# Kernel tuning notes

Measured on AMD Instinct MI355X. Metric: run time of the kernel, lower is better.

## Reference

```python
import jax, jax.numpy as jnp
import numpy as np

STATE_DIM = 16
CHANNELS = 256
LENGTH = 8192
SAMPLE_RATE = 100.0


def setup_inputs() -> dict:
    key = jax.random.key(0)
    ks = jax.random.split(key, 4)
    fan = 1.0 / np.sqrt(CHANNELS)  # lecun-normal-ish scale, flax Dense default
    x = jax.random.normal(ks[0], (LENGTH, CHANNELS), dtype=jnp.float32)
    logA = jnp.log(1.0 + jnp.arange(STATE_DIM, dtype=jnp.float32))  # module's Ainit
    W_dt = jax.random.normal(ks[1], (CHANNELS, CHANNELS), dtype=jnp.float32) * fan
    b_dt = jnp.zeros((CHANNELS,), dtype=jnp.float32)
    W_B = jax.random.normal(ks[2], (CHANNELS, STATE_DIM), dtype=jnp.float32) * fan
    b_B = jnp.zeros((STATE_DIM,), dtype=jnp.float32)
    W_C = jax.random.normal(ks[3], (CHANNELS, STATE_DIM), dtype=jnp.float32) * fan
    b_C = jnp.zeros((STATE_DIM,), dtype=jnp.float32)
    return {"x": x, "logA": logA, "W_dt": W_dt, "b_dt": b_dt,
            "W_B": W_B, "b_B": b_B, "W_C": W_C, "b_C": b_C}


def reference(x, logA, W_dt, b_dt, W_B, b_B, W_C, b_C):
    # x: (L, C)
    A = -jnp.exp(logA)                                   # (S,)
    dt = jax.nn.softplus(1.0 / SAMPLE_RATE + x @ W_dt + b_dt)  # (L, C)
    B = 1.0 + x @ W_B + b_B                              # (L, S)
    C = x @ W_C + b_C                                    # (L, S)
    # discretize: Adiscr = exp(A * dt), shape (L, C, S)
    Adiscr = jnp.exp(dt[:, :, None] * A[None, None, :])
    # Bdiscr = exp((Adiscr - 1) * (B / A))  (faithful to source, incl. outer exp)
    Bdiscr = jnp.exp((Adiscr - 1.0) * (B / A)[:, None, :])  # (L, C, S)
    u = Bdiscr * x[:, :, None]                           # (L, C, S)

    def ssm_scan(p1, p2):
        (A1, c1), (A2, c2) = p1, p2
        return (A2 * A1, c2 + A2 * c1)

    _, h = jax.lax.associative_scan(ssm_scan, (Adiscr, u))  # h: (L, C, S)
    y = jnp.einsum('ls,lcs->lc', C, h)                    # (L, C)
    return y
```

## Files before the change

### kernel.cpp

```cpp
#include <hip/hip_runtime.h>
#include <hip/hip_bf16.h>
#include <math.h>

#define LL 8192
#define CC 256
#define SS 16
#define NJ (CC*SS)
#define GG 256
#define TT 32
#define SP 4
#define CB 64
#define SEGS 16
#define PER (GG/SEGS)

#define LOG2E 1.4426950408889634f
#define LN2   0.6931471805599453f

typedef __attribute__((ext_vector_type(8))) short short8;
typedef __attribute__((ext_vector_type(4))) float floatx4;

__device__ __forceinline__ float fexp2(float v){ return __builtin_amdgcn_exp2f(v); }
__device__ __forceinline__ float flog2v(float v){ return __builtin_amdgcn_logf(v); }

__device__ __forceinline__ float softplus(float z){
    float t = fexp2(-fabsf(z) * LOG2E);
    return fmaxf(z, 0.f) + LN2 * flog2v(1.f + t);
}

__device__ __forceinline__ unsigned short f2b(float f){
    __hip_bfloat16 h = __float2bfloat16(f);
    return *(unsigned short*)&h;
}
__device__ __forceinline__ float b2f(unsigned short u){
    __hip_bfloat16 h = *(__hip_bfloat16*)&u;
    return __bfloat162float(h);
}

#define MBM 64
#define MBN 32
#define MBK 64
#define ASTR 72

__global__ __launch_bounds__(256,4) void k_mm(
    const float* __restrict__ x,
    const float* __restrict__ Wdt, const float* __restrict__ WB,
    const float* __restrict__ WC,
    const float* __restrict__ bdt, const float* __restrict__ bB,
    const float* __restrict__ bC, const float* __restrict__ logA,
    float* __restrict__ dt, float* __restrict__ boa, float* __restrict__ cm)
{
    __shared__ unsigned short Ah[MBM*ASTR];
    __shared__ unsigned short Al[MBM*ASTR];
    __shared__ unsigned short Bh[MBN*ASTR];
    __shared__ unsigned short Bl[MBN*ASTR];

    const int tid  = threadIdx.x;
    const int row0 = blockIdx.x * MBM;
    const int n0   = blockIdx.y * MBN;

    const int lane = tid & 63;
    const int wv   = tid >> 6;
    const int wm   = wv >> 1;
    const int wn   = wv & 1;
    const int m16  = lane & 15;
    const int q    = lane >> 4;

    const int bn  = tid & 31;
    const int bkb = (tid >> 5) * 8;
    const int bcol = n0 + bn;
    const float* __restrict__ wp;
    int wstride;
    if (bcol < 256)      { wp = Wdt + bcol;       wstride = CC; }
    else if (bcol < 272) { wp = WB  + (bcol-256); wstride = SS; }
    else                 { wp = WC  + (bcol-272); wstride = SS; }

    floatx4 acc[2];
    acc[0] = (floatx4){0.f,0.f,0.f,0.f};
    acc[1] = (floatx4){0.f,0.f,0.f,0.f};

    for (int k0 = 0; k0 < CC; k0 += MBK) {
        __syncthreads();
        #pragma unroll
        for (int h2 = 0; h2 < 2; h2++){
            int chunk = tid + h2*256;
            int r    = chunk >> 3;
            int koff = (chunk & 7) * 8;
            float4 f0 = *(const float4*)&x[(size_t)(row0+r)*CC + k0 + koff];
            float4 f1 = *(const float4*)&x[(size_t)(row0+r)*CC + k0 + koff + 4];
            float fv[8] = {f0.x,f0.y,f0.z,f0.w,f1.x,f1.y,f1.z,f1.w};
            unsigned short hs[8], ls[8];
            #pragma unroll
            for (int i=0;i<8;i++){
                hs[i] = f2b(fv[i]);
                ls[i] = f2b(fv[i] - b2f(hs[i]));
            }
            uint4 ph, pl;
            ph.x = (unsigned)hs[0] | ((unsigned)hs[1] << 16);
            ph.y = (unsigned)hs[2] | ((unsigned)hs[3] << 16);
            ph.z = (unsigned)hs[4] | ((unsigned)hs[5] << 16);
            ph.w = (unsigned)hs[6] | ((unsigned)hs[7] << 16);
            pl.x = (unsigned)ls[0] | ((unsigned)ls[1] << 16);
            pl.y = (unsigned)ls[2] | ((unsigned)ls[3] << 16);
            pl.z = (unsigned)ls[4] | ((unsigned)ls[5] << 16);
            pl.w = (unsigned)ls[6] | ((unsigned)ls[7] << 16);
            *(uint4*)&Ah[r*ASTR + koff] = ph;
            *(uint4*)&Al[r*ASTR + koff] = pl;
        }
        {
            unsigned short hs[8], ls[8];
            #pragma unroll
            for (int i=0;i<8;i++){
                float v = wp[(size_t)(k0 + bkb + i)*wstride];
                hs[i] = f2b(v);
                ls[i] = f2b(v - b2f(hs[i]));
            }
            uint4 ph, pl;
            ph.x = (unsigned)hs[0] | ((unsigned)hs[1] << 16);
            ph.y = (unsigned)hs[2] | ((unsigned)hs[3] << 16);
            ph.z = (unsigned)hs[4] | ((unsigned)hs[5] << 16);
            ph.w = (unsigned)hs[6] | ((unsigned)hs[7] << 16);
            pl.x = (unsigned)ls[0] | ((unsigned)ls[1] << 16);
            pl.y = (unsigned)ls[2] | ((unsigned)ls[3] << 16);
            pl.z = (unsigned)ls[4] | ((unsigned)ls[5] << 16);
            pl.w = (unsigned)ls[6] | ((unsigned)ls[7] << 16);
            *(uint4*)&Bh[bn*ASTR + bkb] = ph;
            *(uint4*)&Bl[bn*ASTR + bkb] = pl;
        }
        __syncthreads();

        #pragma unroll
        for (int ks = 0; ks < MBK; ks += 32) {
            short8 bh = *(const short8*)&Bh[(wn*16 + m16)*ASTR + ks + q*8];
            short8 bl = *(const short8*)&Bl[(wn*16 + m16)*ASTR + ks + q*8];
            #pragma unroll
            for (int mt = 0; mt < 2; mt++){
                short8 ah = *(const short8*)&Ah[(wm*32 + mt*16 + m16)*ASTR + ks + q*8];
                short8 al = *(const short8*)&Al[(wm*32 + mt*16 + m16)*ASTR + ks + q*8];
                acc[mt] = __builtin_amdgcn_mfma_f32_16x16x32_bf16(al, bh, acc[mt], 0, 0, 0);
                acc[mt] = __builtin_amdgcn_mfma_f32_16x16x32_bf16(ah, bl, acc[mt], 0, 0, 0);
                acc[mt] = __builtin_amdgcn_mfma_f32_16x16x32_bf16(ah, bh, acc[mt], 0, 0, 0);
            }
        }
    }

    const int col = n0 + wn*16 + m16;
    if (col < 256) {
        float bias = bdt[col];
        #pragma unroll
        for (int mt = 0; mt < 2; mt++){
            #pragma unroll
            for (int r = 0; r < 4; r++){
                int row = row0 + wm*32 + mt*16 + q*4 + r;
                dt[(size_t)row*CC + col] = softplus(0.01f + acc[mt][r] + bias);
            }
        }
    } else if (col < 272) {
        int s = col - 256;
        float A = -fexp2(logA[s] * LOG2E);
        float sc = LOG2E / A;
        float bias = bB[s];
        #pragma unroll
        for (int mt = 0; mt < 2; mt++){
            #pragma unroll
            for (int r = 0; r < 4; r++){
                int row = row0 + wm*32 + mt*16 + q*4 + r;
                boa[(size_t)row*SS + s] = (1.f + acc[mt][r] + bias) * sc;
            }
        }
    } else {
        int s = col - 272;
        float bias = bC[s];
        #pragma unroll
        for (int mt = 0; mt < 2; mt++){
            #pragma unroll
            for (int r = 0; r < 4; r++){
                int row = row0 + wm*32 + mt*16 + q*4 + r;
                cm[(size_t)row*SS + s] = acc[mt][r] + bias;
            }
        }
    }
}

__global__ __launch_bounds__(256) void k_scan1(const float* __restrict__ dt,
    const float* __restrict__ x, const float* __restrict__ boa,
    const float* __restrict__ logA,
    float* __restrict__ Ap, float* __restrict__ Hl)
{
    const int tid = threadIdx.x;
    const int sg  = tid & 3;
    const int cl  = tid >> 2;
    const int g   = blockIdx.x;
    const int c   = blockIdx.y * CB + cl;
    const int row0 = g * TT;

    float Al2[SP];
    #pragma unroll
    for (int i=0;i<SP;i++) Al2[i] = -fexp2(logA[sg*SP+i]*LOG2E) * LOG2E;

    const float* __restrict__ dp = dt  + (size_t)row0*CC + c;
    const float* __restrict__ xp = x   + (size_t)row0*CC + c;
    const float* __restrict__ bp = boa + (size_t)row0*SS + sg*SP;

    float Apr[SP], h[SP];
    #pragma unroll
    for (int i=0;i<SP;i++){ Apr[i]=1.f; h[i]=0.f; }

    #pragma unroll 8
    for (int t=0;t<TT;t++){
        float d  = dp[(size_t)t*CC];
        float xv = xp[(size_t)t*CC];
        float4 bo = *(const float4*)&bp[(size_t)t*SS];
        float bov[SP] = {bo.x, bo.y, bo.z, bo.w};
        #pragma unroll
        for (int s=0;s<SP;s++){
            float a = fexp2(d * Al2[s]);
            float u = fexp2(fmaf(a, bov[s], -bov[s])) * xv;
            h[s] = fmaf(a, h[s], u);
            Apr[s] *= a;
        }
    }

    const size_t base = (size_t)g*NJ + (size_t)c*SS + sg*SP;
    *(float4*)&Ap[base] = make_float4(Apr[0],Apr[1],Apr[2],Apr[3]);
    *(float4*)&Hl[base] = make_float4(h[0],h[1],h[2],h[3]);
}

__global__ __launch_bounds__(256) void k_carry(const float* __restrict__ Ap,
    const float* __restrict__ Hl, float* __restrict__ Cr)
{
    const int tid = threadIdx.x;
    const int jl  = tid & 15;
    const int seg = tid >> 4;
    const int j   = blockIdx.x * 16 + jl;

    const size_t base = (size_t)(seg*PER)*NJ + j;

    float a[PER], u[PER];
    #pragma unroll
    for (int k=0;k<PER;k++){
        a[k] = Ap[base + (size_t)k*NJ];
        u[k] = Hl[base + (size_t)k*NJ];
    }
    float Aag = 1.f, Uag = 0.f;
    #pragma unroll
    for (int k=0;k<PER;k++){ Uag = fmaf(a[k], Uag, u[k]); Aag *= a[k]; }

    __shared__ float As[SEGS][17], Us[SEGS][17];
    As[seg][jl] = Aag; Us[seg][jl] = Uag;
    __syncthreads();
    float hin = 0.f;
    for (int t = 0; t < seg; ++t)
        hin = fmaf(As[t][jl], hin, Us[t][jl]);

    float h = hin;
    #pragma unroll
    for (int k=0;k<PER;k++){
        Cr[base + (size_t)k*NJ] = h;
        h = fmaf(a[k], h, u[k]);
    }
}

__global__ __launch_bounds__(256) void k_scan2(const float* __restrict__ dt,
    const float* __restrict__ x, const float* __restrict__ boa,
    const float* __restrict__ cmat, const float* __restrict__ logA,
    const float* __restrict__ Cr, float* __restrict__ y)
{
    const int tid = threadIdx.x;
    const int sg  = tid & 3;
    const int cl  = tid >> 2;
    const int g   = blockIdx.x;
    const int c   = blockIdx.y * CB + cl;
    const int row0 = g * TT;

    float Al2[SP];
    #pragma unroll
    for (int i=0;i<SP;i++) Al2[i] = -fexp2(logA[sg*SP+i]*LOG2E) * LOG2E;

    const float* __restrict__ dp = dt   + (size_t)row0*CC + c;
    const float* __restrict__ xp = x    + (size_t)row0*CC + c;
    const float* __restrict__ bp = boa  + (size_t)row0*SS + sg*SP;
    const float* __restrict__ cp = cmat + (size_t)row0*SS + sg*SP;
    float* __restrict__ yp = y + (size_t)row0*CC + c;

    float h[SP];
    {
        float4 hc = *(const float4*)&Cr[(size_t)g*NJ + (size_t)c*SS + sg*SP];
        h[0]=hc.x; h[1]=hc.y; h[2]=hc.z; h[3]=hc.w;
    }

    #pragma unroll 8
    for (int t=0;t<TT;t++){
        float d  = dp[(size_t)t*CC];
        float xv = xp[(size_t)t*CC];
        float4 bo = *(const float4*)&bp[(size_t)t*SS];
        float4 cv = *(const float4*)&cp[(size_t)t*SS];
        float bov[SP] = {bo.x,bo.y,bo.z,bo.w};
        float cvv[SP] = {cv.x,cv.y,cv.z,cv.w};
        float yv = 0.f;
        #pragma unroll
        for (int s=0;s<SP;s++){
            float a = fexp2(d * Al2[s]);
            float u = fexp2(fmaf(a, bov[s], -bov[s])) * xv;
            h[s] = fmaf(a, h[s], u);
            yv = fmaf(cvv[s], h[s], yv);
        }
        yv += __shfl_xor(yv, 1);
        yv += __shfl_xor(yv, 2);
        if (sg == 0) yp[(size_t)t*CC] = yv;
    }
}

extern "C" void kernel_launch(void* const* d_in, const int* in_sizes, int n_in,
                              void* d_out, int out_size, void* d_ws, size_t ws_size,
                              hipStream_t stream) {
    const float* x    = (const float*)d_in[0];
    const float* logA = (const float*)d_in[1];
    const float* W_dt = (const float*)d_in[2];
    const float* b_dt = (const float*)d_in[3];
    const float* W_B  = (const float*)d_in[4];
    const float* b_B  = (const float*)d_in[5];
    const float* W_C  = (const float*)d_in[6];
    const float* b_C  = (const float*)d_in[7];
    float* y  = (float*)d_out;
    float* ws = (float*)d_ws;

    float* dt   = ws;
    float* boa  = dt   + (size_t)LL*CC;
    float* cmv  = boa  + (size_t)LL*SS;
    float* Ap   = cmv  + (size_t)LL*SS;
    float* Hl   = Ap   + (size_t)GG*NJ;
    float* Cr   = Hl   + (size_t)GG*NJ;

    hipLaunchKernelGGL(k_mm,   dim3(128,9), dim3(256), 0, stream,
                       x, W_dt, W_B, W_C, b_dt, b_B, b_C, logA, dt, boa, cmv);
    hipLaunchKernelGGL(k_scan1, dim3(GG,4), dim3(256), 0, stream,
                       dt, x, boa, logA, Ap, Hl);
    hipLaunchKernelGGL(k_carry, dim3(NJ/16), dim3(256), 0, stream, Ap, Hl, Cr);
    hipLaunchKernelGGL(k_scan2, dim3(GG,4), dim3(256), 0, stream,
                       dt, x, boa, cmv, logA, Cr, y);
}
```

Measured before the change: 121.7 us.

## Fuse projection GEMM, chunk scans and carry into one cooperative kernel

Replaces the four launches (GEMM, chunk scan, carry propagation, output scan) with a single cooperative kernel of 256 blocks. Each block computes its 32-row slice of dt, B and C into shared memory and never writes them to global memory. Grid-wide syncs separate the chunk scan, carry and final scan phases. This removes the global round trips for dt/boa/cm and the launch gaps, but every block now reconverts all of W into bf16 hi/lo (a 256-fold redundant weight conversion), uses large shared memory, and runs only 256 blocks.

```diff
diff --git a/kernel.cpp b/kernel.cpp
--- a/kernel.cpp
+++ b/kernel.cpp
@@ -1,5 +1,6 @@
 #include <hip/hip_runtime.h>
 #include <hip/hip_bf16.h>
+#include <hip/hip_cooperative_groups.h>
 #include <math.h>
 
 #define LL 8192
@@ -8,13 +9,16 @@
 #define NJ (CC*SS)
 #define GG 256
 #define TT 32
-#define SP 4
-#define CB 64
+#define THREADS 512
 #define SEGS 16
 #define PER (GG/SEGS)
 
 #define LOG2E 1.4426950408889634f
 #define LN2   0.6931471805599453f
+
+#define XSTR 264
+#define WSTR 264
+#define DSTR 260
 
 typedef __attribute__((ext_vector_type(8))) short short8;
 typedef __attribute__((ext_vector_type(4))) float floatx4;
@@ -36,277 +40,228 @@
     return __bfloat162float(h);
 }
 
-#define MBM 64
-#define MBN 32
-#define MBK 64
-#define ASTR 72
-
-__global__ __launch_bounds__(256,4) void k_mm(
-    const float* __restrict__ x,
-    const float* __restrict__ Wdt, const float* __restrict__ WB,
-    const float* __restrict__ WC,
-    const float* __restrict__ bdt, const float* __restrict__ bB,
-    const float* __restrict__ bC, const float* __restrict__ logA,
-    float* __restrict__ dt, float* __restrict__ boa, float* __restrict__ cm)
+__global__ __launch_bounds__(THREADS, 2) void k_fused(
+    const float* __restrict__ x, const float* __restrict__ logA,
+    const float* __restrict__ Wdt, const float* __restrict__ bdt,
+    const float* __restrict__ WB,  const float* __restrict__ bB,
+    const float* __restrict__ WC,  const float* __restrict__ bC,
+    float* __restrict__ Ap, float* __restrict__ Hl, float* __restrict__ Cr,
+    float* __restrict__ y)
 {
-    __shared__ unsigned short Ah[MBM*ASTR];
-    __shared__ unsigned short Al[MBM*ASTR];
-    __shared__ unsigned short Bh[MBN*ASTR];
-    __shared__ unsigned short Bl[MBN*ASTR];
+    __shared__ unsigned short xh[32*XSTR];
+    __shared__ unsigned short xl[32*XSTR];
+    __shared__ unsigned short Wh2[64*WSTR];
+    __shared__ unsigned short Wl2[64*WSTR];
+    __shared__ float dtS[32*DSTR];
+    __shared__ float boaS[32*SS];
+    __shared__ float cmS[32*SS];
+    __shared__ float As[SEGS][17], Us[SEGS][17];
 
     const int tid  = threadIdx.x;
-    const int row0 = blockIdx.x * MBM;
-    const int n0   = blockIdx.y * MBN;
+    const int g    = blockIdx.x;
+    const int row0 = g * TT;
+
+    #pragma unroll
+    for (int j = 0; j < 4; j++){
+        int idx = tid + j*THREADS;
+        int r   = idx >> 6;
+        int kq  = (idx & 63) * 4;
+        float4 f = *(const float4*)&x[(size_t)(row0+r)*CC + kq];
+        float fv[4] = {f.x, f.y, f.z, f.w};
+        unsigned short hs[4], ls[4];
+        #pragma unroll
+        for (int i=0;i<4;i++){ hs[i]=f2b(fv[i]); ls[i]=f2b(fv[i]-b2f(hs[i])); }
+        uint2 ph, pl;
+        ph.x = (unsigned)hs[0] | ((unsigned)hs[1] << 16);
+        ph.y = (unsigned)hs[2] | ((unsigned)hs[3] << 16);
+        pl.x = (unsigned)ls[0] | ((unsigned)ls[1] << 16);
+        pl.y = (unsigned)ls[2] | ((unsigned)ls[3] << 16);
+        *(uint2*)&xh[r*XSTR + kq] = ph;
+        *(uint2*)&xl[r*XSTR + kq] = pl;
+    }
 
     const int lane = tid & 63;
     const int wv   = tid >> 6;
-    const int wm   = wv >> 1;
-    const int wn   = wv & 1;
     const int m16  = lane & 15;
     const int q    = lane >> 4;
-
-    const int bn  = tid & 31;
-    const int bkb = (tid >> 5) * 8;
-    const int bcol = n0 + bn;
-    const float* __restrict__ wp;
-    int wstride;
-    if (bcol < 256)      { wp = Wdt + bcol;       wstride = CC; }
-    else if (bcol < 272) { wp = WB  + (bcol-256); wstride = SS; }
-    else                 { wp = WC  + (bcol-272); wstride = SS; }
-
-    floatx4 acc[2];
-    acc[0] = (floatx4){0.f,0.f,0.f,0.f};
-    acc[1] = (floatx4){0.f,0.f,0.f,0.f};
-
-    for (int k0 = 0; k0 < CC; k0 += MBK) {
+    const int mi   = wv & 1;
+    const int ni   = wv >> 1;
+
+    const int cw = tid & 63;
+    const int kb = (tid >> 6) * 32;
+
+    for (int nt = 0; nt < 5; nt++){
+        {
+            int bcol = nt*64 + cw;
+            const float* wp = nullptr; int wstr = 0;
+            if (bcol < 256)      { wp = Wdt + bcol;       wstr = CC; }
+            else if (bcol < 272) { wp = WB  + (bcol-256); wstr = SS; }
+            else if (bcol < 288) { wp = WC  + (bcol-272); wstr = SS; }
+            if (wp){
+                #pragma unroll
+                for (int i8 = 0; i8 < 32; i8 += 8){
+                    unsigned short hs[8], ls[8];
+                    #pragma unroll
+                    for (int u = 0; u < 8; u++){
+                        float v = wp[(size_t)(kb+i8+u)*wstr];
+                        hs[u] = f2b(v);
+                        ls[u] = f2b(v - b2f(hs[u]));
+                    }
+                    uint4 ph, pl;
+                    ph.x = (unsigned)hs[0] | ((unsigned)hs[1] << 16);
+                    ph.y = (unsigned)hs[2] | ((unsigned)hs[3] << 16);
+                    ph.z = (unsigned)hs[4] | ((unsigned)hs[5] << 16);
+                    ph.w = (unsigned)hs[6] | ((unsigned)hs[7] << 16);
+                    pl.x = (unsigned)ls[0] | ((unsigned)ls[1] << 16);
+                    pl.y = (unsigned)ls[2] | ((unsigned)ls[3] << 16);
+                    pl.z = (unsigned)ls[4] | ((unsigned)ls[5] << 16);
+                    pl.w = (unsigned)ls[6] | ((unsigned)ls[7] << 16);
+                    *(uint4*)&Wh2[cw*WSTR + kb + i8] = ph;
+                    *(uint4*)&Wl2[cw*WSTR + kb + i8] = pl;
+                }
+            }
+        }
         __syncthreads();
-        #pragma unroll
-        for (int h2 = 0; h2 < 2; h2++){
-            int chunk = tid + h2*256;
-            int r    = chunk >> 3;
-            int koff = (chunk & 7) * 8;
-            float4 f0 = *(const float4*)&x[(size_t)(row0+r)*CC + k0 + koff];
-            float4 f1 = *(const float4*)&x[(size_t)(row0+r)*CC + k0 + koff + 4];
-            float fv[8] = {f0.x,f0.y,f0.z,f0.w,f1.x,f1.y,f1.z,f1.w};
-            unsigned short hs[8], ls[8];
+
+        if (nt < 4 || ni < 2){
+            floatx4 acc = (floatx4){0.f,0.f,0.f,0.f};
             #pragma unroll
-            for (int i=0;i<8;i++){
-                hs[i] = f2b(fv[i]);
-                ls[i] = f2b(fv[i] - b2f(hs[i]));
+            for (int ks = 0; ks < 256; ks += 32){
+                short8 bh = *(const short8*)&Wh2[(ni*16+m16)*WSTR + ks + q*8];
+                short8 bl = *(const short8*)&Wl2[(ni*16+m16)*WSTR + ks + q*8];
+                short8 ah = *(const short8*)&xh [(mi*16+m16)*XSTR + ks + q*8];
+                short8 al = *(const short8*)&xl [(mi*16+m16)*XSTR + ks + q*8];
+                acc = __builtin_amdgcn_mfma_f32_16x16x32_bf16(al, bh, acc, 0, 0, 0);
+                acc = __builtin_amdgcn_mfma_f32_16x16x32_bf16(ah, bl, acc, 0, 0, 0);
+                acc = __builtin_amdgcn_mfma_f32_16x16x32_bf16(ah, bh, acc, 0, 0, 0);
             }
-            uint4 ph, pl;
-            ph.x = (unsigned)hs[0] | ((unsigned)hs[1] << 16);
-            ph.y = (unsigned)hs[2] | ((unsigned)hs[3] << 16);
-            ph.z = (unsigned)hs[4] | ((unsigned)hs[5] << 16);
-            ph.w = (unsigned)hs[6] | ((unsigned)hs[7] << 16);
-            pl.x = (unsigned)ls[0] | ((unsigned)ls[1] << 16);
-            pl.y = (unsigned)ls[2] | ((unsigned)ls[3] << 16);
-            pl.z = (unsigned)ls[4] | ((unsigned)ls[5] << 16);
-            pl.w = (unsigned)ls[6] | ((unsigned)ls[7] << 16);
-            *(uint4*)&Ah[r*ASTR + koff] = ph;
-            *(uint4*)&Al[r*ASTR + koff] = pl;
-        }
-        {
-            unsigned short hs[8], ls[8];
-            #pragma unroll
-            for (int i=0;i<8;i++){
-                float v = wp[(size_t)(k0 + bkb + i)*wstride];
-                hs[i] = f2b(v);
-                ls[i] = f2b(v - b2f(hs[i]));
+            int col   = nt*64 + ni*16 + m16;
+            int rbase = mi*16 + q*4;
+            if (col < 256){
+                float bias = bdt[col];
+                #pragma unroll
+                for (int r=0;r<4;r++)
+                    dtS[(rbase+r)*DSTR + col] = softplus(0.01f + acc[r] + bias);
+            } else if (col < 272){
+                int s = col - 256;
+                float A  = -fexp2(logA[s]*LOG2E);
+                float sc = LOG2E / A;
+                float bias = bB[s];
+                #pragma unroll
+                for (int r=0;r<4;r++)
+                    boaS[(rbase+r)*SS + s] = (1.f + acc[r] + bias) * sc;
+            } else {
+                int s = col - 272;
+                float bias = bC[s];
+                #pragma unroll
+                for (int r=0;r<4;r++)
+                    cmS[(rbase+r)*SS + s] = acc[r] + bias;
             }
-            uint4 ph, pl;
-            ph.x = (unsigned)hs[0] | ((unsigned)hs[1] << 16);
-            ph.y = (unsigned)hs[2] | ((unsigned)hs[3] << 16);
-            ph.z = (unsigned)hs[4] | ((unsigned)hs[5] << 16);
-            ph.w = (unsigned)hs[6] | ((unsigned)hs[7] << 16);
-            pl.x = (unsigned)ls[0] | ((unsigned)ls[1] << 16);
-            pl.y = (unsigned)ls[2] | ((unsigned)ls[3] << 16);
-            pl.z = (unsigned)ls[4] | ((unsigned)ls[5] << 16);
-            pl.w = (unsigned)ls[6] | ((unsigned)ls[7] << 16);
-            *(uint4*)&Bh[bn*ASTR + bkb] = ph;
-            *(uint4*)&Bl[bn*ASTR + bkb] = pl;
         }
         __syncthreads();
-
-        #pragma unroll
-        for (int ks = 0; ks < MBK; ks += 32) {
-            short8 bh = *(const short8*)&Bh[(wn*16 + m16)*ASTR + ks + q*8];
-            short8 bl = *(const short8*)&Bl[(wn*16 + m16)*ASTR + ks + q*8];
-            #pragma unroll
-            for (int mt = 0; mt < 2; mt++){
-                short8 ah = *(const short8*)&Ah[(wm*32 + mt*16 + m16)*ASTR + ks + q*8];
-                short8 al = *(const short8*)&Al[(wm*32 + mt*16 + m16)*ASTR + ks + q*8];
-                acc[mt] = __builtin_amdgcn_mfma_f32_16x16x32_bf16(al, bh, acc[mt], 0, 0, 0);
-                acc[mt] = __builtin_amdgcn_mfma_f32_16x16x32_bf16(ah, bl, acc[mt], 0, 0, 0);
-                acc[mt] = __builtin_amdgcn_mfma_f32_16x16x32_bf16(ah, bh, acc[mt], 0, 0, 0);
-            }
-        }
-    }
-
-    const int col = n0 + wn*16 + m16;
-    if (col < 256) {
-        float bias = bdt[col];
-        #pragma unroll
-        for (int mt = 0; mt < 2; mt++){
-            #pragma unroll
-            for (int r = 0; r < 4; r++){
-                int row = row0 + wm*32 + mt*16 + q*4 + r;
-                dt[(size_t)row*CC + col] = softplus(0.01f + acc[mt][r] + bias);
-            }
-        }
-    } else if (col < 272) {
-        int s = col - 256;
-        float A = -fexp2(logA[s] * LOG2E);
-        float sc = LOG2E / A;
-        float bias = bB[s];
-        #pragma unroll
-        for (int mt = 0; mt < 2; mt++){
-            #pragma unroll
-            for (int r = 0; r < 4; r++){
-                int row = row0 + wm*32 + mt*16 + q*4 + r;
-                boa[(size_t)row*SS + s] = (1.f + acc[mt][r] + bias) * sc;
-            }
-        }
-    } else {
-        int s = col - 272;
-        float bias = bC[s];
-        #pragma unroll
-        for (int mt = 0; mt < 2; mt++){
-            #pragma unroll
-            for (int r = 0; r < 4; r++){
-                int row = row0 + wm*32 + mt*16 + q*4 + r;
-                cm[(size_t)row*SS + s] = acc[mt][r] + bias;
-            }
-        }
-    }
-}
-
-__global__ __launch_bounds__(256) void k_scan1(const float* __restrict__ dt,
-    const float* __restrict__ x, const float* __restrict__ boa,
-    const float* __restrict__ logA,
-    float* __restrict__ Ap, float* __restrict__ Hl)
-{
-    const int tid = threadIdx.x;
-    const int sg  = tid & 3;
-    const int cl  = tid >> 2;
-    const int g   = blockIdx.x;
-    const int c   = blockIdx.y * CB + cl;
-    const int row0 = g * TT;
-
-    float Al2[SP];
-    #pragma unroll
-    for (int i=0;i<SP;i++) Al2[i] = -fexp2(logA[sg*SP+i]*LOG2E) * LOG2E;
-
-    const float* __restrict__ dp = dt  + (size_t)row0*CC + c;
-    const float* __restrict__ xp = x   + (size_t)row0*CC + c;
-    const float* __restrict__ bp = boa + (size_t)row0*SS + sg*SP;
-
-    float Apr[SP], h[SP];
-    #pragma unroll
-    for (int i=0;i<SP;i++){ Apr[i]=1.f; h[i]=0.f; }
-
-    #pragma unroll 8
+    }
+
+    const int c  = tid >> 1;
+    const int sb = (tid & 1) * 8;
+
+    float Al2v[8];
+    #pragma unroll
+    for (int i=0;i<8;i++) Al2v[i] = -fexp2(logA[sb+i]*LOG2E) * LOG2E;
+
+    float xr[TT];
+    #pragma unroll
+    for (int t=0;t<TT;t++) xr[t] = x[(size_t)(row0+t)*CC + c];
+
+    float Apr[8], h[8];
+    #pragma unroll
+    for (int i=0;i<8;i++){ Apr[i]=1.f; h[i]=0.f; }
+
+    #pragma unroll 4
     for (int t=0;t<TT;t++){
-        float d  = dp[(size_t)t*CC];
-        float xv = xp[(size_t)t*CC];
-        float4 bo = *(const float4*)&bp[(size_t)t*SS];
-        float bov[SP] = {bo.x, bo.y, bo.z, bo.w};
-        #pragma unroll
-        for (int s=0;s<SP;s++){
-            float a = fexp2(d * Al2[s]);
-            float u = fexp2(fmaf(a, bov[s], -bov[s])) * xv;
+        float d  = dtS[t*DSTR + c];
+        float4 b0 = *(const float4*)&boaS[t*SS + sb];
+        float4 b1 = *(const float4*)&boaS[t*SS + sb + 4];
+        float bo[8] = {b0.x,b0.y,b0.z,b0.w,b1.x,b1.y,b1.z,b1.w};
+        #pragma unroll
+        for (int s=0;s<8;s++){
+            float a = fexp2(d * Al2v[s]);
+            float u = fexp2(fmaf(a, bo[s], -bo[s])) * xr[t];
             h[s] = fmaf(a, h[s], u);
             Apr[s] *= a;
         }
     }
-
-    const size_t base = (size_t)g*NJ + (size_t)c*SS + sg*SP;
-    *(float4*)&Ap[base] = make_float4(Apr[0],Apr[1],Apr[2],Apr[3]);
-    *(float4*)&Hl[base] = make_float4(h[0],h[1],h[2],h[3]);
-}
-
-__global__ __launch_bounds__(256) void k_carry(const float* __restrict__ Ap,
-    const float* __restrict__ Hl, float* __restrict__ Cr)
-{
-    const int tid = threadIdx.x;
+    {
+        const size_t base = (size_t)g*NJ + (size_t)c*SS + sb;
+        *(float4*)&Ap[base]   = make_float4(Apr[0],Apr[1],Apr[2],Apr[3]);
+        *(float4*)&Ap[base+4] = make_float4(Apr[4],Apr[5],Apr[6],Apr[7]);
+        *(float4*)&Hl[base]   = make_float4(h[0],h[1],h[2],h[3]);
+        *(float4*)&Hl[base+4] = make_float4(h[4],h[5],h[6],h[7]);
+    }
+
+    __threadfence();
+    cooperative_groups::this_grid().sync();
+    __threadfence();
+
+    float a2[PER], u2[PER];
     const int jl  = tid & 15;
-    const int seg = tid >> 4;
-    const int j   = blockIdx.x * 16 + jl;
-
-    const size_t base = (size_t)(seg*PER)*NJ + j;
-
-    float a[PER], u[PER];
-    #pragma unroll
-    for (int k=0;k<PER;k++){
-        a[k] = Ap[base + (size_t)k*NJ];
-        u[k] = Hl[base + (size_t)k*NJ];
-    }
-    float Aag = 1.f, Uag = 0.f;
-    #pragma unroll
-    for (int k=0;k<PER;k++){ Uag = fmaf(a[k], Uag, u[k]); Aag *= a[k]; }
-
-    __shared__ float As[SEGS][17], Us[SEGS][17];
-    As[seg][jl] = Aag; Us[seg][jl] = Uag;
+    const int seg = (tid >> 4) & 15;
+    const size_t cb = (size_t)(seg*PER)*NJ + (size_t)(g*16 + jl);
+    if (tid < 256){
+        #pragma unroll
+        for (int k=0;k<PER;k++){
+            a2[k] = Ap[cb + (size_t)k*NJ];
+            u2[k] = Hl[cb + (size_t)k*NJ];
+        }
+        float Aag = 1.f, Uag = 0.f;
+        #pragma unroll
+        for (int k=0;k<PER;k++){ Uag = fmaf(a2[k], Uag, u2[k]); Aag *= a2[k]; }
+        As[seg][jl] = Aag; Us[seg][jl] = Uag;
+    }
     __syncthreads();
-    float hin = 0.f;
-    for (int t = 0; t < seg; ++t)
-        hin = fmaf(As[t][jl], hin, Us[t][jl]);
-
-    float h = hin;
-    #pragma unroll
-    for (int k=0;k<PER;k++){
-        Cr[base + (size_t)k*NJ] = h;
-        h = fmaf(a[k], h, u[k]);
-    }
-}
-
-__global__ __launch_bounds__(256) void k_scan2(const float* __restrict__ dt,
-    const float* __restrict__ x, const float* __restrict__ boa,
-    const float* __restrict__ cmat, const float* __restrict__ logA,
-    const float* __restrict__ Cr, float* __restrict__ y)
-{
-    const int tid = threadIdx.x;
-    const int sg  = tid & 3;
-    const int cl  = tid >> 2;
-    const int g   = blockIdx.x;
-    const int c   = blockIdx.y * CB + cl;
-    const int row0 = g * TT;
-
-    float Al2[SP];
-    #pragma unroll
-    for (int i=0;i<SP;i++) Al2[i] = -fexp2(logA[sg*SP+i]*LOG2E) * LOG2E;
-
-    const float* __restrict__ dp = dt   + (size_t)row0*CC + c;
-    const float* __restrict__ xp = x    + (size_t)row0*CC + c;
-    const float* __restrict__ bp = boa  + (size_t)row0*SS + sg*SP;
-    const float* __restrict__ cp = cmat + (size_t)row0*SS + sg*SP;
-    float* __restrict__ yp = y + (size_t)row0*CC + c;
-
-    float h[SP];
+    if (tid < 256){
+        float hin = 0.f;
+        for (int t2 = 0; t2 < seg; ++t2)
+            hin = fmaf(As[t2][jl], hin, Us[t2][jl]);
+        float hh = hin;
+        #pragma unroll
+        for (int k=0;k<PER;k++){
+            Cr[cb + (size_t)k*NJ] = hh;
+            hh = fmaf(a2[k], hh, u2[k]);
+        }
+    }
+
+    __threadfence();
+    cooperative_groups::this_grid().sync();
+    __threadfence();
+
+    float hh[8];
     {
-        float4 hc = *(const float4*)&Cr[(size_t)g*NJ + (size_t)c*SS + sg*SP];
-        h[0]=hc.x; h[1]=hc.y; h[2]=hc.z; h[3]=hc.w;
-    }
-
-    #pragma unroll 8
+        const size_t base = (size_t)g*NJ + (size_t)c*SS + sb;
+        float4 h0 = *(const float4*)&Cr[base];
+        float4 h1 = *(const float4*)&Cr[base+4];
+        hh[0]=h0.x; hh[1]=h0.y; hh[2]=h0.z; hh[3]=h0.w;
+        hh[4]=h1.x; hh[5]=h1.y; hh[6]=h1.z; hh[7]=h1.w;
+    }
+
+    #pragma unroll 4
     for (int t=0;t<TT;t++){
-        float d  = dp[(size_t)t*CC];
-        float xv = xp[(size_t)t*CC];
-        float4 bo = *(const float4*)&bp[(size_t)t*SS];
-        float4 cv = *(const float4*)&cp[(size_t)t*SS];
-        float bov[SP] = {bo.x,bo.y,bo.z,bo.w};
-        float cvv[SP] = {cv.x,cv.y,cv.z,cv.w};
+        float d  = dtS[t*DSTR + c];
+        float4 b0 = *(const float4*)&boaS[t*SS + sb];
+        float4 b1 = *(const float4*)&boaS[t*SS + sb + 4];
+        float4 c0 = *(const float4*)&cmS [t*SS + sb];
+        float4 c1 = *(const float4*)&cmS [t*SS + sb + 4];
+        float bo[8] = {b0.x,b0.y,b0.z,b0.w,b1.x,b1.y,b1.z,b1.w};
+        float cv[8] = {c0.x,c0.y,c0.z,c0.w,c1.x,c1.y,c1.z,c1.w};
         float yv = 0.f;
         #pragma unroll
-        for (int s=0;s<SP;s++){
-            float a = fexp2(d * Al2[s]);
-            float u = fexp2(fmaf(a, bov[s], -bov[s])) * xv;
-            h[s] = fmaf(a, h[s], u);
-            yv = fmaf(cvv[s], h[s], yv);
+        for (int s=0;s<8;s++){
+            float a = fexp2(d * Al2v[s]);
+            float u = fexp2(fmaf(a, bo[s], -bo[s])) * xr[t];
+            hh[s] = fmaf(a, hh[s], u);
+            yv = fmaf(cv[s], hh[s], yv);
         }
         yv += __shfl_xor(yv, 1);
-        yv += __shfl_xor(yv, 2);
-        if (sg == 0) yp[(size_t)t*CC] = yv;
+        if ((tid & 1) == 0) y[(size_t)(row0+t)*CC + c] = yv;
     }
 }
 
@@ -324,18 +279,17 @@
     float* y  = (float*)d_out;
     float* ws = (float*)d_ws;
 
-    float* dt   = ws;
-    float* boa  = dt   + (size_t)LL*CC;
-    float* cmv  = boa  + (size_t)LL*SS;
-    float* Ap   = cmv  + (size_t)LL*SS;
-    float* Hl   = Ap   + (size_t)GG*NJ;
-    float* Cr   = Hl   + (size_t)GG*NJ;
-
-    hipLaunchKernelGGL(k_mm,   dim3(128,9), dim3(256), 0, stream,
-                       x, W_dt, W_B, W_C, b_dt, b_B, b_C, logA, dt, boa, cmv);
-    hipLaunchKernelGGL(k_scan1, dim3(GG,4), dim3(256), 0, stream,
-                       dt, x, boa, logA, Ap, Hl);
-    hipLaunchKernelGGL(k_carry, dim3(NJ/16), dim3(256), 0, stream, Ap, Hl, Cr);
-    hipLaunchKernelGGL(k_scan2, dim3(GG,4), dim3(256), 0, stream,
-                       dt, x, boa, cmv, logA, Cr, y);
-}
+    float* Ap = ws;
+    float* Hl = Ap + (size_t)GG*NJ;
+    float* Cr = Hl + (size_t)GG*NJ;
+
+    void* args[] = {
+        (void*)&x, (void*)&logA,
+        (void*)&W_dt, (void*)&b_dt,
+        (void*)&W_B, (void*)&b_B,
+        (void*)&W_C, (void*)&b_C,
+        (void*)&Ap, (void*)&Hl, (void*)&Cr, (void*)&y
+    };
+    hipLaunchCooperativeKernel((void*)k_fused, dim3(GG), dim3(THREADS),
+                               args, 0, stream);
+}
```

New measurement: 365.8 us. 200% more time.
